# Kernel optimization log

Hardware: AMD Instinct MI355X
Metric: run time of the kernel (lower is better)

## Reference

```python
import jax, jax.numpy as jnp
import numpy as np
from jax import lax


def _conv2d_same(x, w):
    # x: [B,C,H,W], w: [O,C,3,3], padding=1 -> [B,O,H,W]
    return lax.conv_general_dilated(
        x, w, window_strides=(1, 1), padding=((1, 1), (1, 1)),
        dimension_numbers=("NCHW", "OIHW", "NCHW"))


def setup_inputs() -> dict:
    key = jax.random.key(0)
    k1, k2, k3 = jax.random.split(key, 3)
    B, C, H, W = 8, 3, 1024, 512   # W == c_in
    d_model = 512
    x = jax.random.normal(k1, (B, C, H, W), dtype=jnp.float32)
    # Conv1d(c_in, d_model, k=3) weight/bias (kaiming-ish scale)
    w_out = jax.random.normal(k2, (d_model, W, 3), dtype=jnp.float32) * (1.0 / np.sqrt(W * 3).astype(np.float32))
    b_out = jax.random.normal(k3, (d_model,), dtype=jnp.float32) * 0.01
    return {"x": x, "w_out": w_out, "b_out": b_out}


def reference(x, w_out, b_out):
    B, C, H, W = x.shape
    # fixed (non-trainable) kernels, exactly as in the torch module
    ave_k = jnp.full((1, C, 3, 3), 1.0 / 9.0, dtype=jnp.float32)      # [1,C,3,3] -> out_ch 1
    g = jnp.array([[1/16, 1/8, 1/16], [1/8, 1/4, 1/8], [1/16, 1/8, 1/16]], dtype=jnp.float32)
    gau_k = jnp.broadcast_to(g, (1, C, 3, 3))

    # per-sample fftn over (C,H,W) == batched fftn over axes 1..3
    F = jnp.fft.fftn(x, axes=(1, 2, 3))                               # complex64 [B,C,H,W]
    amp = jnp.abs(F) + jnp.float32(np.exp(-10.0))
    log_amp = jnp.log(amp)
    phase = jnp.angle(F)

    amp_filter = _conv2d_same(log_amp, ave_k)                         # [B,1,H,W]
    amp_sr = log_amp - amp_filter                                     # broadcast -> [B,C,H,W]

    SR = jnp.abs(jnp.fft.ifftn(jnp.exp(amp_sr + 1j * phase), axes=(1, 2, 3)))
    SR = _conv2d_same(SR, gau_k)                                      # [B,1,H,W]

    # threshold at per-sample mean (loop in torch was per batch element)
    mean = jnp.mean(SR, axis=(1, 2, 3), keepdims=True)
    SR = jnp.where(SR > mean, SR, jnp.float32(0.0))

    Y = SR[:, 0]                                                      # [B,H,W]
    Y = jnp.transpose(Y, (0, 2, 1))                                   # [B,W,H]
    # Conv1d(c_in, d_model, k=3, padding=1, padding_mode='circular')
    Yp = jnp.pad(Y, ((0, 0), (0, 0), (1, 1)), mode="wrap")
    out = lax.conv_general_dilated(
        Yp, w_out, window_strides=(1,), padding=((0, 0),),
        dimension_numbers=("NCH", "OIH", "NCH"))                      # [B,d_model,H]
    out = out + b_out[None, :, None]
    return jnp.transpose(out, (0, 2, 1))                              # [B,H,d_model]
```

## Files before the change

kernel.cpp:

```cpp
#include <hip/hip_runtime.h>
#include <math.h>

#define TPB 256

constexpr int Bn = 8, Cn = 3, Hn = 1024, Wn = 512;
constexpr long long HWn  = (long long)Hn * Wn;
constexpr long long CHWn = (long long)Cn * HWn;
constexpr float INV_NTOT = 1.0f / (float)(Cn * Hn * Wn);
constexpr float EPS10 = 4.5399929762484854e-05f;
constexpr float S3 = 0.86602540378443864676f;

#define SWZ(x) ((x) + ((x) >> 3))

__global__ __launch_bounds__(TPB) void k_fft_wc_fwd(const float* __restrict__ x,
                                                    float2* __restrict__ F) {
    __shared__ float sre[3][576], sim[3][576], twc[256], tws[256];
    int rb = blockIdx.x;
    int b = rb >> 10, h = rb & 1023;
    const float* xb = x + (long long)b * CHWn + (long long)h * Wn;
    float2* Fb = F + (long long)b * CHWn + (long long)h * Wn;
    int t = threadIdx.x;

    {   float s, c;
        sincospif(-2.0f * (float)t / (float)Wn, &s, &c);
        twc[t] = c; tws[t] = s; }
    for (int i = t; i < Wn; i += TPB) {
        int j = SWZ(__brev((unsigned)i) >> (32 - 9));
        #pragma unroll
        for (int ch = 0; ch < 3; ch++) {
            sre[ch][j] = xb[ch * HWn + i];
            sim[ch][j] = 0.0f;
        }
    }
    __syncthreads();
    #pragma unroll
    for (int st = 0; st < 9; st++) {
        int half = 1 << st;
        int blk = t >> st, j = t & (half - 1);
        int pos = (blk << (st + 1)) + j;
        float c = twc[j << (8 - st)], s = tws[j << (8 - st)];
        int p0 = SWZ(pos), p1 = SWZ(pos + half);
        #pragma unroll
        for (int ch = 0; ch < 3; ch++) {
            float ure = sre[ch][p0], uim = sim[ch][p0];
            float vre = sre[ch][p1], vim = sim[ch][p1];
            float tre = vre * c - vim * s, tim = vre * s + vim * c;
            sre[ch][p0] = ure + tre;  sim[ch][p0] = uim + tim;
            sre[ch][p1] = ure - tre;  sim[ch][p1] = uim - tim;
        }
        __syncthreads();
    }
    for (int i = t; i < Wn; i += TPB) {
        int a = SWZ(i);
        float x0 = sre[0][a], y0 = sim[0][a];
        float x1 = sre[1][a], y1 = sim[1][a];
        float x2 = sre[2][a], y2 = sim[2][a];
        float sx = x1 + x2, sy = y1 + y2, dx = x1 - x2, dy = y1 - y2;
        Fb[i]           = make_float2(x0 + sx, y0 + sy);
        Fb[HWn + i]     = make_float2(x0 - 0.5f * sx + S3 * dy, y0 - 0.5f * sy - S3 * dx);
        Fb[2 * HWn + i] = make_float2(x0 - 0.5f * sx - S3 * dy, y0 - 0.5f * sy + S3 * dx);
    }
}

__global__ __launch_bounds__(TPB) void k_ifft_wc_abs(const float2* __restrict__ F,
                                                     float* __restrict__ SRabs) {
    __shared__ float sre[3][576], sim[3][576], twc[256], tws[256];
    int rb = blockIdx.x;
    int b = rb >> 10, h = rb & 1023;
    const float2* Fb = F + (long long)b * CHWn + (long long)h * Wn;
    float* ob = SRabs + (long long)b * CHWn + (long long)h * Wn;
    int t = threadIdx.x;

    {   float s, c;
        sincospif(2.0f * (float)t / (float)Wn, &s, &c);
        twc[t] = c; tws[t] = s; }
    for (int i = t; i < Wn; i += TPB) {
        float2 z0 = Fb[i], z1 = Fb[HWn + i], z2 = Fb[2 * HWn + i];
        float sx = z1.x + z2.x, sy = z1.y + z2.y;
        float dx = z1.x - z2.x, dy = z1.y - z2.y;
        int j = SWZ(__brev((unsigned)i) >> (32 - 9));
        sre[0][j] = z0.x + sx;                 sim[0][j] = z0.y + sy;
        sre[1][j] = z0.x - 0.5f * sx - S3 * dy; sim[1][j] = z0.y - 0.5f * sy + S3 * dx;
        sre[2][j] = z0.x - 0.5f * sx + S3 * dy; sim[2][j] = z0.y - 0.5f * sy - S3 * dx;
    }
    __syncthreads();
    #pragma unroll
    for (int st = 0; st < 9; st++) {
        int half = 1 << st;
        int blk = t >> st, j = t & (half - 1);
        int pos = (blk << (st + 1)) + j;
        float c = twc[j << (8 - st)], s = tws[j << (8 - st)];
        int p0 = SWZ(pos), p1 = SWZ(pos + half);
        #pragma unroll
        for (int ch = 0; ch < 3; ch++) {
            float ure = sre[ch][p0], uim = sim[ch][p0];
            float vre = sre[ch][p1], vim = sim[ch][p1];
            float tre = vre * c - vim * s, tim = vre * s + vim * c;
            sre[ch][p0] = ure + tre;  sim[ch][p0] = uim + tim;
            sre[ch][p1] = ure - tre;  sim[ch][p1] = uim - tim;
        }
        __syncthreads();
    }
    for (int i = t; i < Wn; i += TPB) {
        int a = SWZ(i);
        #pragma unroll
        for (int ch = 0; ch < 3; ch++) {
            float re = sre[ch][a], im = sim[ch][a];
            ob[ch * HWn + i] = sqrtf(re * re + im * im) * INV_NTOT;
        }
    }
}

template <int INV>
__global__ __launch_bounds__(512) void k_fft_h(float2* __restrict__ F,
                                               float* __restrict__ LA,
                                               const float* __restrict__ AF) {
    __shared__ float2 tile[1024][9];
    __shared__ float twc[512], tws[512];
    int bid = blockIdx.x;
    int g  = bid & 63;
    int bc = bid >> 6;
    int p = g & 7, q3 = (g >> 3) & 1, r = g >> 4;
    int wt = ((p + (r << 3)) << 1) | q3;
    int w0 = wt << 3;
    float2* base = F + (long long)bc * HWn + w0;
    float* LAp = LA + (long long)bc * HWn + w0;
    const float* AFb = AF + (long long)(bc / 3) * HWn + w0;
    int t = threadIdx.x;

    {   float s, c;
        sincospif((INV ? 2.0f : -2.0f) * (float)t / (float)Hn, &s, &c);
        twc[t] = c; tws[t] = s; }

    int w = t & 7;
    int d = (t >> 3) & 7;
    #pragma unroll
    for (int k = 0; k < 16; k++) {
        int c8 = (t >> 6) + (k << 3);
        int h = c8 + (d << 7);
        float2 z = base[(long long)h * Wn + w];
        if (INV) {
            float la = LAp[(long long)h * Wn + w];
            float af = AFb[(long long)h * Wn + w];
            float m = expf(la - af);
            float rr = sqrtf(z.x * z.x + z.y * z.y);
            if (rr > 0.0f) { float sc = m / rr; z.x *= sc; z.y *= sc; }
            else           { z.x = m; z.y = 0.0f; }
        }
        int hj = __brev((unsigned)h) >> (32 - 10);
        tile[hj][w] = z;
    }
    __syncthreads();

    for (int st = 0; st < 10; st++) {
        int half = 1 << st;
        #pragma unroll
        for (int qq = 0; qq < 8; qq++) {
            int q = qq * 512 + t;
            int ww = q & 7;
            int i = q >> 3;
            int blk = i >> st, j = i & (half - 1);
            int pos = (blk << (st + 1)) + j;
            float c = twc[j << (9 - st)], s = tws[j << (9 - st)];
            float2 u = tile[pos][ww];
            float2 v = tile[pos + half][ww];
            float tre = v.x * c - v.y * s;
            float tim = v.x * s + v.y * c;
            tile[pos][ww]        = make_float2(u.x + tre, u.y + tim);
            tile[pos + half][ww] = make_float2(u.x - tre, u.y - tim);
        }
        __syncthreads();
    }

    #pragma unroll
    for (int k = 0; k < 16; k++) {
        int grp = (t >> 6) + (k << 3);
        int h = (grp << 3) | ((t >> 3) & 7);
        float2 z = tile[h][w];
        base[(long long)h * Wn + w] = z;
        if (!INV) {
            LAp[(long long)h * Wn + w] =
                logf(sqrtf(z.x * z.x + z.y * z.y) + EPS10);
        }
    }
}

template <int GAU>
__global__ __launch_bounds__(TPB) void k_conv3x3(const float* __restrict__ src,
                                                 float* __restrict__ dst,
                                                 float* __restrict__ part) {
    __shared__ float tile[3][10][140];
    int w0 = blockIdx.x << 7;
    int h0 = blockIdx.y << 3;
    int b  = blockIdx.z;
    int t  = threadIdx.x;

    for (int i = t; i < 1020; i += TPB) {
        int c = i / 340, rem = i - c * 340;
        int hh = rem / 34, w4 = rem - hh * 34;
        int h  = h0 + hh - 1;
        int gw = w0 - 4 + (w4 << 2);
        float4 v = make_float4(0.f, 0.f, 0.f, 0.f);
        if ((unsigned)h < (unsigned)Hn && (unsigned)gw <= 508u)
            v = *(const float4*)(src + ((long long)(b * 3 + c)) * HWn +
                                 (long long)h * Wn + gw);
        *(float4*)&tile[c][hh][w4 << 2] = v;
    }
    __syncthreads();

    const float K = GAU ? 2.0f : 1.0f;
    const float norm = GAU ? (1.0f / 16.0f) : (1.0f / 9.0f);
    int hh = t >> 5;
    int wb = (t & 31) << 2;
    float o0 = 0.f, o1 = 0.f, o2 = 0.f, o3 = 0.f;
    #pragma unroll
    for (int c = 0; c < 3; c++)
        #pragma unroll
        for (int dh = 0; dh < 3; dh++) {
            const float* row = &tile[c][hh + dh][3 + wb];
            float a0 = row[0], a1 = row[1], a2 = row[2],
                  a3 = row[3], a4 = row[4], a5 = row[5];
            float vw = (dh == 1) ? K : 1.0f;
            o0 += vw * (a0 + K * a1 + a2);
            o1 += vw * (a1 + K * a2 + a3);
            o2 += vw * (a2 + K * a3 + a4);
            o3 += vw * (a3 + K * a4 + a5);
        }
    o0 *= norm; o1 *= norm; o2 *= norm; o3 *= norm;
    *(float4*)(dst + (long long)b * HWn + (long long)(h0 + hh) * Wn + w0 + wb)
        = make_float4(o0, o1, o2, o3);

    if (GAU) {
        float s = o0 + o1 + o2 + o3;
        #pragma unroll
        for (int o = 32; o > 0; o >>= 1) s += __shfl_down(s, o);
        __shared__ float ls[4];
        if ((t & 63) == 0) ls[t >> 6] = s;
        __syncthreads();
        if (t == 0)
            part[((long long)b << 9) + (blockIdx.y << 2) + blockIdx.x]
                = ls[0] + ls[1] + ls[2] + ls[3];
    }
}

__global__ __launch_bounds__(TPB) void k_mean_final(const float* __restrict__ part,
                                                    float* __restrict__ mean) {
    int b = blockIdx.x;
    int t = threadIdx.x;
    float s = part[(b << 9) + t] + part[(b << 9) + 256 + t];
    #pragma unroll
    for (int o = 32; o > 0; o >>= 1) s += __shfl_down(s, o);
    __shared__ float ls[4];
    if ((t & 63) == 0) ls[t >> 6] = s;
    __syncthreads();
    if (t == 0)
        mean[b] = (ls[0] + ls[1] + ls[2] + ls[3]) * (1.0f / (float)HWn);
}

__global__ __launch_bounds__(TPB) void k_outgemm(const float* __restrict__ SRg,
                                                 const float* __restrict__ meanv,
                                                 const float* __restrict__ w_out,
                                                 const float* __restrict__ b_out,
                                                 float* __restrict__ out) {
    __shared__ __align__(16) float As[32][68];
    __shared__ __align__(16) float Bs[3][32][64];
    int o0 = blockIdx.x << 6;
    int h0 = blockIdx.y << 6;
    int b = blockIdx.z;
    int t = threadIdx.x;
    int to = t & 15, th = t >> 4;
    float meanb = meanv[b];
    const float* srb = SRg + (long long)b * HWn;

    float acc[4][4];
    #pragma unroll
    for (int i = 0; i < 4; i++)
        #pragma unroll
        for (int j = 0; j < 4; j++) acc[i][j] = 0.0f;

    for (int w0 = 0; w0 < Wn; w0 += 32) {
        for (int i = t; i < 66 * 32; i += TPB) {
            int r = i >> 5, wc = i & 31;
            int h = (h0 - 1 + r) & (Hn - 1);
            float v = srb[(long long)h * Wn + w0 + wc];
            As[wc][r] = (v > meanb) ? v : 0.0f;
        }
        {
            int oo = t & 63, g = t >> 6;
            const float4* wpv = (const float4*)(w_out +
                (long long)(o0 + oo) * 1536 + (long long)w0 * 3 + g * 24);
            #pragma unroll
            for (int j2 = 0; j2 < 6; j2++) {
                float4 v4 = wpv[j2];
                int mm = j2 * 4;
                Bs[(mm) % 3][g * 8 + (mm) / 3][oo]         = v4.x;
                Bs[(mm + 1) % 3][g * 8 + (mm + 1) / 3][oo] = v4.y;
                Bs[(mm + 2) % 3][g * 8 + (mm + 2) / 3][oo] = v4.z;
                Bs[(mm + 3) % 3][g * 8 + (mm + 3) / 3][oo] = v4.w;
            }
        }
        __syncthreads();
        for (int w = 0; w < 32; w++) {
            float4 a03 = *(const float4*)&As[w][th << 2];
            float2 a45 = *(const float2*)&As[w][(th << 2) + 4];
            float a[6] = {a03.x, a03.y, a03.z, a03.w, a45.x, a45.y};
            #pragma unroll
            for (int k = 0; k < 3; k++) {
                float4 bv = *(const float4*)&Bs[k][w][to << 2];
                #pragma unroll
                for (int i2 = 0; i2 < 4; i2++) {
                    acc[i2][0] += a[i2 + k] * bv.x;
                    acc[i2][1] += a[i2 + k] * bv.y;
                    acc[i2][2] += a[i2 + k] * bv.z;
                    acc[i2][3] += a[i2 + k] * bv.w;
                }
            }
        }
        __syncthreads();
    }

    float4 bias = *(const float4*)&b_out[o0 + (to << 2)];
    #pragma unroll
    for (int i2 = 0; i2 < 4; i2++) {
        int h = h0 + (th << 2) + i2;
        float4 v = make_float4(acc[i2][0] + bias.x, acc[i2][1] + bias.y,
                               acc[i2][2] + bias.z, acc[i2][3] + bias.w);
        *(float4*)&out[((long long)b * Hn + h) * 512 + o0 + (to << 2)] = v;
    }
}

extern "C" void kernel_launch(void* const* d_in, const int* in_sizes, int n_in,
                              void* d_out, int out_size, void* d_ws, size_t ws_size,
                              hipStream_t stream) {
    (void)in_sizes; (void)n_in; (void)out_size;
    const float* x     = (const float*)d_in[0];
    const float* w_out = (const float*)d_in[1];
    const float* b_out = (const float*)d_in[2];
    float* out = (float*)d_out;

    const size_t CBUF_BYTES = (size_t)Bn * CHWn * sizeof(float2);
    const size_t LA_BYTES   = (size_t)Bn * CHWn * sizeof(float);
    const size_t AF_BYTES   = (size_t)Bn * HWn * sizeof(float);
    const size_t NEED = CBUF_BYTES + LA_BYTES + AF_BYTES + 64 + 4096 * sizeof(float);
    if (ws_size < NEED) return;

    char* ws = (char*)d_ws;
    float2* CBUF = (float2*)ws;
    float*  LA   = (float*)(ws + CBUF_BYTES);
    float*  AF   = (float*)(ws + CBUF_BYTES + LA_BYTES);
    float*  MEAN = (float*)(ws + CBUF_BYTES + LA_BYTES + AF_BYTES);
    float*  PART = (float*)(ws + CBUF_BYTES + LA_BYTES + AF_BYTES + 64);

    k_fft_wc_fwd<<<Bn * Hn, TPB, 0, stream>>>(x, CBUF);
    k_fft_h<0><<<Bn * Cn * 64, 512, 0, stream>>>(CBUF, LA, nullptr);

    k_conv3x3<0><<<dim3(4, 128, 8), TPB, 0, stream>>>(LA, AF, nullptr);

    k_fft_h<1><<<Bn * Cn * 64, 512, 0, stream>>>(CBUF, LA, AF);
    k_ifft_wc_abs<<<Bn * Hn, TPB, 0, stream>>>(CBUF, LA);

    k_conv3x3<1><<<dim3(4, 128, 8), TPB, 0, stream>>>(LA, AF, PART);
    k_mean_final<<<8, TPB, 0, stream>>>(PART, MEAN);
    k_outgemm<<<dim3(8, 16, Bn), TPB, 0, stream>>>(AF, MEAN, w_out, b_out, out);
}
```

Measured before the change: 596.5 us.

## Enlarge output GEMM tile to 128x128 with 8x8 per-thread register blocking

The circular Conv1d GEMM kernel now computes a 128x128 (h, o) tile per block instead of 64x64, and each thread holds four 4x4 accumulator quadrants. This raises arithmetic intensity per shared-memory load and halves the redundant halo and weight loads across blocks. In exchange it uses more registers and LDS per block, and the grid shrinks from 1024 to 256 blocks, which may underfill the GPU's CUs.

```diff
diff --git a/kernel.cpp b/kernel.cpp
--- a/kernel.cpp
+++ b/kernel.cpp
@@ -262,70 +262,95 @@
                                                  const float* __restrict__ w_out,
                                                  const float* __restrict__ b_out,
                                                  float* __restrict__ out) {
-    __shared__ __align__(16) float As[32][68];
-    __shared__ __align__(16) float Bs[3][32][64];
-    int o0 = blockIdx.x << 6;
-    int h0 = blockIdx.y << 6;
+    __shared__ __align__(16) float As[32][132];
+    __shared__ __align__(16) float Bs[3][32][128];
+    int o0 = blockIdx.x << 7;
+    int h0 = blockIdx.y << 7;
     int b = blockIdx.z;
     int t = threadIdx.x;
     int to = t & 15, th = t >> 4;
     float meanb = meanv[b];
     const float* srb = SRg + (long long)b * HWn;
 
-    float acc[4][4];
+    float a_ll[4][4], a_lh[4][4], a_hl[4][4], a_hh[4][4];
     #pragma unroll
     for (int i = 0; i < 4; i++)
         #pragma unroll
-        for (int j = 0; j < 4; j++) acc[i][j] = 0.0f;
+        for (int j = 0; j < 4; j++) {
+            a_ll[i][j] = 0.0f; a_lh[i][j] = 0.0f;
+            a_hl[i][j] = 0.0f; a_hh[i][j] = 0.0f;
+        }
 
     for (int w0 = 0; w0 < Wn; w0 += 32) {
-        for (int i = t; i < 66 * 32; i += TPB) {
+        for (int i = t; i < 130 * 32; i += TPB) {
             int r = i >> 5, wc = i & 31;
             int h = (h0 - 1 + r) & (Hn - 1);
             float v = srb[(long long)h * Wn + w0 + wc];
             As[wc][r] = (v > meanb) ? v : 0.0f;
         }
         {
-            int oo = t & 63, g = t >> 6;
+            int oo = t & 127, g = t >> 7;
             const float4* wpv = (const float4*)(w_out +
-                (long long)(o0 + oo) * 1536 + (long long)w0 * 3 + g * 24);
+                (long long)(o0 + oo) * 1536 + (long long)(w0 + g * 16) * 3);
             #pragma unroll
-            for (int j2 = 0; j2 < 6; j2++) {
+            for (int j2 = 0; j2 < 12; j2++) {
                 float4 v4 = wpv[j2];
                 int mm = j2 * 4;
-                Bs[(mm) % 3][g * 8 + (mm) / 3][oo]         = v4.x;
-                Bs[(mm + 1) % 3][g * 8 + (mm + 1) / 3][oo] = v4.y;
-                Bs[(mm + 2) % 3][g * 8 + (mm + 2) / 3][oo] = v4.z;
-                Bs[(mm + 3) % 3][g * 8 + (mm + 3) / 3][oo] = v4.w;
+                Bs[(mm) % 3][g * 16 + (mm) / 3][oo]         = v4.x;
+                Bs[(mm + 1) % 3][g * 16 + (mm + 1) / 3][oo] = v4.y;
+                Bs[(mm + 2) % 3][g * 16 + (mm + 2) / 3][oo] = v4.z;
+                Bs[(mm + 3) % 3][g * 16 + (mm + 3) / 3][oo] = v4.w;
             }
         }
         __syncthreads();
         for (int w = 0; w < 32; w++) {
-            float4 a03 = *(const float4*)&As[w][th << 2];
-            float2 a45 = *(const float2*)&As[w][(th << 2) + 4];
-            float a[6] = {a03.x, a03.y, a03.z, a03.w, a45.x, a45.y};
+            float4 al0 = *(const float4*)&As[w][th << 2];
+            float2 al1 = *(const float2*)&As[w][(th << 2) + 4];
+            float4 ah0 = *(const float4*)&As[w][64 + (th << 2)];
+            float2 ah1 = *(const float2*)&As[w][64 + (th << 2) + 4];
+            float alo[6] = {al0.x, al0.y, al0.z, al0.w, al1.x, al1.y};
+            float ahi[6] = {ah0.x, ah0.y, ah0.z, ah0.w, ah1.x, ah1.y};
             #pragma unroll
             for (int k = 0; k < 3; k++) {
-                float4 bv = *(const float4*)&Bs[k][w][to << 2];
+                float4 bl = *(const float4*)&Bs[k][w][to << 2];
+                float4 bh = *(const float4*)&Bs[k][w][64 + (to << 2)];
                 #pragma unroll
                 for (int i2 = 0; i2 < 4; i2++) {
-                    acc[i2][0] += a[i2 + k] * bv.x;
-                    acc[i2][1] += a[i2 + k] * bv.y;
-                    acc[i2][2] += a[i2 + k] * bv.z;
-                    acc[i2][3] += a[i2 + k] * bv.w;
+                    float fl = alo[i2 + k], fh = ahi[i2 + k];
+                    a_ll[i2][0] += fl * bl.x;  a_ll[i2][1] += fl * bl.y;
+                    a_ll[i2][2] += fl * bl.z;  a_ll[i2][3] += fl * bl.w;
+                    a_lh[i2][0] += fl * bh.x;  a_lh[i2][1] += fl * bh.y;
+                    a_lh[i2][2] += fl * bh.z;  a_lh[i2][3] += fl * bh.w;
+                    a_hl[i2][0] += fh * bl.x;  a_hl[i2][1] += fh * bl.y;
+                    a_hl[i2][2] += fh * bl.z;  a_hl[i2][3] += fh * bl.w;
+                    a_hh[i2][0] += fh * bh.x;  a_hh[i2][1] += fh * bh.y;
+                    a_hh[i2][2] += fh * bh.z;  a_hh[i2][3] += fh * bh.w;
                 }
             }
         }
         __syncthreads();
     }
 
-    float4 bias = *(const float4*)&b_out[o0 + (to << 2)];
+    float4 bias_l = *(const float4*)&b_out[o0 + (to << 2)];
+    float4 bias_h = *(const float4*)&b_out[o0 + 64 + (to << 2)];
     #pragma unroll
     for (int i2 = 0; i2 < 4; i2++) {
-        int h = h0 + (th << 2) + i2;
-        float4 v = make_float4(acc[i2][0] + bias.x, acc[i2][1] + bias.y,
-                               acc[i2][2] + bias.z, acc[i2][3] + bias.w);
-        *(float4*)&out[((long long)b * Hn + h) * 512 + o0 + (to << 2)] = v;
+        int hl = h0 + (th << 2) + i2;
+        int hh2 = hl + 64;
+        float* rowl = &out[((long long)b * Hn + hl) * 512 + o0];
+        float* rowh = &out[((long long)b * Hn + hh2) * 512 + o0];
+        *(float4*)&rowl[to << 2] = make_float4(
+            a_ll[i2][0] + bias_l.x, a_ll[i2][1] + bias_l.y,
+            a_ll[i2][2] + bias_l.z, a_ll[i2][3] + bias_l.w);
+        *(float4*)&rowl[64 + (to << 2)] = make_float4(
+            a_lh[i2][0] + bias_h.x, a_lh[i2][1] + bias_h.y,
+            a_lh[i2][2] + bias_h.z, a_lh[i2][3] + bias_h.w);
+        *(float4*)&rowh[to << 2] = make_float4(
+            a_hl[i2][0] + bias_l.x, a_hl[i2][1] + bias_l.y,
+            a_hl[i2][2] + bias_l.z, a_hl[i2][3] + bias_l.w);
+        *(float4*)&rowh[64 + (to << 2)] = make_float4(
+            a_hh[i2][0] + bias_h.x, a_hh[i2][1] + bias_h.y,
+            a_hh[i2][2] + bias_h.z, a_hh[i2][3] + bias_h.w);
     }
 }
 
@@ -361,5 +386,5 @@
 
     k_conv3x3<1><<<dim3(4, 128, 8), TPB, 0, stream>>>(LA, AF, PART);
     k_mean_final<<<8, TPB, 0, stream>>>(PART, MEAN);
-    k_outgemm<<<dim3(8, 16, Bn), TPB, 0, stream>>>(AF, MEAN, w_out, b_out, out);
-}
+    k_outgemm<<<dim3(4, 8, Bn), TPB, 0, stream>>>(AF, MEAN, w_out, b_out, out);
+}
```

New measurement: 619.2 us. 1.04x slower.
